# Kernel tuning notes

Hardware: AMD Instinct MI355X
Metric: run time of the kernel (lower is better)

Reference implementation:

```python
import jax, jax.numpy as jnp
import numpy as np

N_HEADS = 8
CLIP = 10.0  # tanh clipping constant of the pointer logits
NEG = -1e9


def setup_inputs() -> dict:
    key = jax.random.key(0)
    ks = jax.random.split(key, 10)
    B, N, H = 1024, 100, 128
    s = 1.0 / np.sqrt(H).astype(np.float32)
    return {
        "encoder_inputs": jax.random.normal(ks[0], (B, N, H), jnp.float32),
        "pool": jax.random.normal(ks[1], (B, H), jnp.float32),
        "capacity": jnp.full((B, 1), 50.0, jnp.float32),  # vehicle capacity
        "demand": (1.0 + 9.0 * jax.random.uniform(ks[2], (B, N), jnp.float32)).at[:, 0].set(0.0),  # depot demand = 0
        "fc_w": jax.random.normal(ks[3], (H, H + 1), jnp.float32) * s,
        "fc1_w": jax.random.normal(ks[4], (H, H), jnp.float32) * s,
        "Wq": jax.random.normal(ks[5], (H, H), jnp.float32) * s,
        "Wk": jax.random.normal(ks[6], (H, H), jnp.float32) * s,
        "Wv": jax.random.normal(ks[7], (H, H), jnp.float32) * s,
        "Wo": jax.random.normal(ks[8], (H, H), jnp.float32) * s,
        "Wk2": jax.random.normal(ks[9], (H, H), jnp.float32) * s,
        "n_steps": 128,
        "T": 1,
        "greedy": 1,
    }


def _decode(encoder_inputs, pool, capacity, demand, fc_w, fc1_w, Wq, Wk, Wv, Wo, Wk2, n_steps, T):
    B, N, H = encoder_inputs.shape
    hd = H // N_HEADS
    # encoder projections are step-invariant -> hoist out of the loop
    K = (encoder_inputs @ Wk.T).reshape(B, N, N_HEADS, hd)
    V = (encoder_inputs @ Wv.T).reshape(B, N, N_HEADS, hd)
    K2 = encoder_inputs @ Wk2.T  # [B, N, H] pointer keys
    pool_proj = pool @ fc1_w.T   # [B, H]
    base_cap = capacity[0, 0]
    rows = jnp.arange(B)

    def update_mask(cap, index, mask1):
        # mask1: permanently visited customers (depot never permanently masked)
        go_depot = (index == 0)
        mask1 = mask1.at[rows, index].set(1.0)
        mask1 = mask1.at[:, 0].set(0.0)
        mask = jnp.maximum(mask1, (demand > cap).astype(jnp.float32))
        # cannot stay at depot; but depot must stay open once all customers are masked
        all_cust = jnp.all(mask[:, 1:] > 0.0, axis=1)
        depot = jnp.where(all_cust, 0.0, go_depot.astype(jnp.float32))
        mask = mask.at[:, 0].set(depot)
        return mask, mask1

    mask0, mask1_0 = update_mask(capacity, jnp.zeros((B,), jnp.int32), jnp.zeros((B, N), jnp.float32))
    inp0 = encoder_inputs[:, 0, :]
    inv_sqrt_hd = 1.0 / jnp.sqrt(jnp.float32(hd))
    inv_sqrt_h = 1.0 / jnp.sqrt(jnp.float32(H))

    def step(carry, _):
        _inp, cap, mask, mask1 = carry
        dec = jnp.concatenate([_inp, cap], axis=-1) @ fc_w.T + pool_proj  # [B, H]
        # multi-head glimpse over encoder nodes
        q = (dec @ Wq.T).reshape(B, N_HEADS, hd)
        scores = jnp.einsum('bhd,bnhd->bhn', q, K) * inv_sqrt_hd
        scores = jnp.where(mask[:, None, :] > 0.0, NEG, scores)
        attn = jax.nn.softmax(scores, axis=-1)
        glimpse = jnp.einsum('bhn,bnhd->bhd', attn, V).reshape(B, H) @ Wo.T
        # single-head clipped pointer logits
        u = CLIP * jnp.tanh(jnp.einsum('bh,bnh->bn', glimpse, K2) * inv_sqrt_h)
        u = jnp.where(mask > 0.0, NEG, u)
        logp_all = jax.nn.log_softmax(u / T, axis=-1)
        index = jnp.argmax(logp_all, axis=-1)  # greedy decoding
        log_p = jnp.take_along_axis(logp_all, index[:, None], axis=1)[:, 0]
        is_done = (jnp.sum(mask1[:, 1:], axis=1) >= N - 1).astype(jnp.float32)
        log_p = log_p * (1.0 - is_done)
        # state update: subtract served demand; reset to base capacity at depot
        sel_d = jnp.take_along_axis(demand, index[:, None], axis=1)
        cap = jnp.where(index[:, None] == 0, base_cap, cap - sel_d)
        mask, mask1 = update_mask(cap, index, mask1)
        _inp = jnp.take_along_axis(encoder_inputs, index[:, None, None], axis=1)[:, 0]
        return (_inp, cap, mask, mask1), (index, log_p)

    _, (actions, log_ps) = jax.lax.scan(step, (inp0, capacity, mask0, mask1_0), None, length=n_steps)
    return actions.T, jnp.sum(log_ps, axis=0)  # ([B, n_steps], [B])


def reference(encoder_inputs, pool, capacity, demand, fc_w, fc1_w, Wq, Wk, Wv, Wo, Wk2, n_steps, T, greedy):
    actions, log_p = _decode(encoder_inputs, pool, capacity, demand, fc_w, fc1_w, Wq, Wk, Wv, Wo, Wk2, n_steps, T)
    return actions, log_p
```

## Files before the change

kernel.cpp:

```cpp
#include <hip/hip_runtime.h>
#include <math.h>

#define NNODE 100
#define NEGV  -1000000000.0f

__device__ float g_Wall [128 * 512];
__device__ float g_Wall2[128 * 128];
__device__ float g_qcap [128];
__device__ float g_C    [(size_t)102400 * 512];
__device__ float g_qpool[(size_t)1024 * 128];
__device__ float g_S1   [(size_t)1024 * 100 * 800];
__device__ float g_Scap [(size_t)1024 * 800];

__device__ __forceinline__ float fast_rcp(float x) { return __builtin_amdgcn_rcpf(x); }
__device__ __forceinline__ float tanh10(float z) {
    const float e2 = __expf(2.0f * z);
    return fmaf(-20.0f, __builtin_amdgcn_rcpf(e2 + 1.0f), 10.0f);
}

template<int CTRL>
__device__ __forceinline__ int dpp_i(int v) {
    return __builtin_amdgcn_update_dpp(0, v, CTRL, 0xF, 0xF, true);
}
template<int CTRL>
__device__ __forceinline__ float dpp_f(float v) {
    return __uint_as_float((unsigned)dpp_i<CTRL>(__float_as_int(v)));
}
__device__ __forceinline__ float swz16_f(float v) {
    return __uint_as_float(
        (unsigned)__builtin_amdgcn_ds_swizzle(__float_as_int(v), 0x401F));
}

__global__ __launch_bounds__(128) void prep_kernel(
    const float* __restrict__ Wk,  const float* __restrict__ Wv,
    const float* __restrict__ Wk2, const float* __restrict__ Wo,
    const float* __restrict__ Wq,  const float* __restrict__ fc_w,
    const float* __restrict__ fc1_w)
{
    const int c = blockIdx.x;
    const int k = threadIdx.x;
    if (c < 128) {
        g_Wall[k * 512 + c] = Wk[c * 128 + k];
    } else if (c < 256) {
        g_Wall[k * 512 + c] = Wv[(c - 128) * 128 + k];
    } else if (c < 384) {
        const int cc = c - 256;
        float acc = 0.f;
        for (int h = 0; h < 128; h++)
            acc = fmaf(Wk2[h * 128 + k], Wo[h * 128 + cc], acc);
        g_Wall[k * 512 + c] = acc;
    } else if (c < 512) {
        const int cc = c - 384;
        float acc = 0.f;
        for (int j = 0; j < 128; j++)
            acc = fmaf(Wq[cc * 128 + j], fc_w[j * 129 + k], acc);
        g_Wall[k * 512 + c] = acc;
    } else if (c == 512) {
        float acc = 0.f;
        for (int j = 0; j < 128; j++)
            acc = fmaf(Wq[k * 128 + j], fc_w[j * 129 + 128], acc);
        g_qcap[k] = acc;
    } else {
        const int cc = c - 513;
        float acc = 0.f;
        for (int j = 0; j < 128; j++)
            acc = fmaf(Wq[cc * 128 + j], fc1_w[j * 128 + k], acc);
        g_Wall2[k * 128 + cc] = acc;
    }
}

__global__ __launch_bounds__(256) void gemm_kernel(const float* __restrict__ A,
                                                   int mode)
{
    const float* __restrict__ W = mode ? g_Wall2 : g_Wall;
    float* __restrict__ C       = mode ? g_qpool : g_C;
    const int ncols             = mode ? 128 : 512;
    const int m0 = blockIdx.x * 128, n0 = blockIdx.y * 128;

    __shared__ __align__(16) float At[32 * 132];
    __shared__ __align__(16) float Ws[32 * 128];
    const int tid = threadIdx.x;
    const int tm = tid >> 5, tn = tid & 31;
    const int mb = tm * 16, nb = tn * 4;
    float4 acc[16];
#pragma unroll
    for (int i = 0; i < 16; i++) acc[i] = make_float4(0.f, 0.f, 0.f, 0.f);

    for (int kc = 0; kc < 4; kc++) {
        for (int f = tid; f < 1024; f += 256) {
            const int r = f >> 3, q8 = f & 7;
            float4 a = *(const float4*)&A[(size_t)(m0 + r) * 128 + kc * 32 + q8 * 4];
            At[(q8 * 4 + 0) * 132 + r] = a.x;
            At[(q8 * 4 + 1) * 132 + r] = a.y;
            At[(q8 * 4 + 2) * 132 + r] = a.z;
            At[(q8 * 4 + 3) * 132 + r] = a.w;
            const int kl = f >> 5, q = f & 31;
            *(float4*)&Ws[kl * 128 + q * 4] =
                *(const float4*)&W[(size_t)(kc * 32 + kl) * ncols + n0 + q * 4];
        }
        __syncthreads();
        for (int k = 0; k < 32; k++) {
            const float4 w = *(float4*)&Ws[k * 128 + nb];
#pragma unroll
            for (int i = 0; i < 16; i += 4) {
                const float4 a = *(float4*)&At[k * 132 + mb + i];
                acc[i + 0].x = fmaf(a.x, w.x, acc[i + 0].x);
                acc[i + 0].y = fmaf(a.x, w.y, acc[i + 0].y);
                acc[i + 0].z = fmaf(a.x, w.z, acc[i + 0].z);
                acc[i + 0].w = fmaf(a.x, w.w, acc[i + 0].w);
                acc[i + 1].x = fmaf(a.y, w.x, acc[i + 1].x);
                acc[i + 1].y = fmaf(a.y, w.y, acc[i + 1].y);
                acc[i + 1].z = fmaf(a.y, w.z, acc[i + 1].z);
                acc[i + 1].w = fmaf(a.y, w.w, acc[i + 1].w);
                acc[i + 2].x = fmaf(a.z, w.x, acc[i + 2].x);
                acc[i + 2].y = fmaf(a.z, w.y, acc[i + 2].y);
                acc[i + 2].z = fmaf(a.z, w.z, acc[i + 2].z);
                acc[i + 2].w = fmaf(a.z, w.w, acc[i + 2].w);
                acc[i + 3].x = fmaf(a.w, w.x, acc[i + 3].x);
                acc[i + 3].y = fmaf(a.w, w.y, acc[i + 3].y);
                acc[i + 3].z = fmaf(a.w, w.z, acc[i + 3].z);
                acc[i + 3].w = fmaf(a.w, w.w, acc[i + 3].w);
            }
        }
        __syncthreads();
    }
#pragma unroll
    for (int i = 0; i < 16; i++)
        *(float4*)&C[(size_t)(m0 + mb + i) * ncols + n0 + nb] = acc[i];
}

__global__ __launch_bounds__(256) void s1_kernel()
{
    const int b = blockIdx.x;
    const int tid = threadIdx.x;
    const int h = tid >> 5, l32 = tid & 31;
    const float* __restrict__ Crow = &g_C[(size_t)b * 100 * 512];

    float4 kr[4][4];
    int nn[4];
#pragma unroll
    for (int j = 0; j < 4; j++) {
        nn[j] = l32 + 32 * j;
#pragma unroll
        for (int i = 0; i < 4; i++) {
            kr[j][i] = (nn[j] < 100)
                ? *(const float4*)&Crow[(size_t)nn[j] * 512 + h * 16 + i * 4]
                : make_float4(0.f, 0.f, 0.f, 0.f);
        }
    }
    float4 qc[4], qp[4];
#pragma unroll
    for (int i = 0; i < 4; i++) {
        qc[i] = *(const float4*)&g_qcap[h * 16 + i * 4];
        qp[i] = *(const float4*)&g_qpool[(size_t)b * 128 + h * 16 + i * 4];
    }
    float sp[4];
#pragma unroll
    for (int j = 0; j < 4; j++) {
        float dc = 0.f, dp = 0.f;
#pragma unroll
        for (int i = 0; i < 4; i++) {
            dc = fmaf(kr[j][i].x, qc[i].x, dc); dc = fmaf(kr[j][i].y, qc[i].y, dc);
            dc = fmaf(kr[j][i].z, qc[i].z, dc); dc = fmaf(kr[j][i].w, qc[i].w, dc);
            dp = fmaf(kr[j][i].x, qp[i].x, dp); dp = fmaf(kr[j][i].y, qp[i].y, dp);
            dp = fmaf(kr[j][i].z, qp[i].z, dp); dp = fmaf(kr[j][i].w, qp[i].w, dp);
        }
        sp[j] = dp;
        if (nn[j] < 100)
            g_Scap[(size_t)b * 800 + h * 100 + nn[j]] = dc * 0.25f;
    }

    float* __restrict__ S1b = &g_S1[(size_t)b * 80000];
#pragma unroll 2
    for (int m = 0; m < 100; m++) {
        float4 q[4];
#pragma unroll
        for (int i = 0; i < 4; i++)
            q[i] = *(const float4*)&Crow[(size_t)m * 512 + 384 + h * 16 + i * 4];
#pragma unroll
        for (int j = 0; j < 4; j++) {
            if (nn[j] < 100) {
                float d = 0.f;
#pragma unroll
                for (int i = 0; i < 4; i++) {
                    d = fmaf(kr[j][i].x, q[i].x, d); d = fmaf(kr[j][i].y, q[i].y, d);
                    d = fmaf(kr[j][i].z, q[i].z, d); d = fmaf(kr[j][i].w, q[i].w, d);
                }
                S1b[(size_t)m * 800 + h * 100 + nn[j]] = (d + sp[j]) * 0.25f;
            }
        }
    }
}

__global__ __launch_bounds__(256) void decode_kernel(
    const float* __restrict__ capacity, const float* __restrict__ demand,
    const int* __restrict__ nsteps_p, const int* __restrict__ T_p,
    float* __restrict__ out)
{
    __shared__ float u_buf[800];
    __shared__ float demand_sh[NNODE];
    __shared__ int   act_sh[512];
    __shared__ int   idx_sh;
    __shared__ float lp_sh;

    const int tid = threadIdx.x;
    const int b   = blockIdx.x;
    const int nsteps = nsteps_p[0];
    const float invT = 1.0f / (float)T_p[0];
    const float base_cap = capacity[0];
    const float inv_sqrt_h = 0.08838834764831845f;

    const float4* __restrict__ C4  = (const float4*)&g_C[(size_t)b * 100 * 512];
    const float*  __restrict__ S1b = &g_S1[(size_t)b * 80000];

    const int w = tid >> 6, l = tid & 63;
    const int g = l >> 3, f = l & 7;
    const int F = 8 * w + f;
    const int h8 = tid >> 5, l32 = tid & 31;

    float4 Vreg[13], K2r[13];
#pragma unroll
    for (int m = 0; m < 13; m++) {
        const int n = g + 8 * m;
        const bool v = n < 100;
        Vreg[m] = v ? C4[(size_t)n * 128 + 32 + F] : make_float4(0.f, 0.f, 0.f, 0.f);
        K2r[m]  = v ? C4[(size_t)n * 128 + 64 + F] : make_float4(0.f, 0.f, 0.f, 0.f);
    }
    float s1r[4], scapr[4], d4[4];
#pragma unroll
    for (int j = 0; j < 4; j++) {
        const int nj = l32 + 32 * j;
        const bool v = nj < 100;
        scapr[j] = v ? g_Scap[(size_t)b * 800 + h8 * 100 + nj] : 0.f;
        s1r[j]   = v ? S1b[h8 * 100 + nj] : 0.f;
        d4[j]    = v ? demand[b * 100 + nj] : 1.0e30f;
    }
    const float de0 = demand[b * 100 + l];
    const float de1 = (l + 64 < 100) ? demand[b * 100 + l + 64] : 1.0e30f;
    for (int n = tid; n < 100; n += 256) demand_sh[n] = demand[b * 100 + n];
    for (int t = tid; t < 512; t += 256) act_sh[t] = 0;
    bool me0 = false, me1 = false;
    unsigned mb4 = 0;
    float cap_r = capacity[b];
    float depot_r;
    {
        const bool am0 = (l == 0) ? true : (de0 > cap_r);
        const bool am1 = (l + 64 >= 100) ? true : (de1 > cap_r);
        depot_r = __all(am0 && am1) ? 0.f : 1.f;
    }
    float logp_r = 0.f;
    int visited_r = 0;
    __syncthreads();

    for (int s = 0; s < nsteps; s++) {
        const float cap = cap_r;

        float a[4];
        float tot;
        {
            float sc[4];
#pragma unroll
            for (int j = 0; j < 4; j++) {
                const int nj = l32 + 32 * j;
                const bool m = (nj == 0) ? (depot_r != 0.f)
                    : (((mb4 >> j) & 1u) || (d4[j] > cap));
                const float raw = fmaf(cap, scapr[j], s1r[j]);
                sc[j] = (nj < 100 && !m) ? raw : NEGV;
            }
#pragma unroll
            for (int j = 0; j < 4; j++) a[j] = __expf(sc[j]);
            tot = (a[0] + a[1]) + (a[2] + a[3]);
        }

        float4 gp4 = make_float4(0.f, 0.f, 0.f, 0.f);
#pragma unroll
        for (int m = 0; m < 13; m++) {
            const int src = ((f >> 2) << 5) | (8 * (m & 3) + g);
            const float av = __shfl(a[m >> 2], src, 64);
            gp4.x = fmaf(av, Vreg[m].x, gp4.x);
            gp4.y = fmaf(av, Vreg[m].y, gp4.y);
            gp4.z = fmaf(av, Vreg[m].z, gp4.z);
            gp4.w = fmaf(av, Vreg[m].w, gp4.w);
        }
        tot += dpp_f<0xB1>(tot);
        tot += dpp_f<0x4E>(tot);
        tot += dpp_f<0x124>(tot);
        tot += dpp_f<0x128>(tot);
        tot += swz16_f(tot);
        gp4.x += dpp_f<0x128>(gp4.x);
        gp4.y += dpp_f<0x128>(gp4.y);
        gp4.z += dpp_f<0x128>(gp4.z);
        gp4.w += dpp_f<0x128>(gp4.w);
        gp4.x += swz16_f(gp4.x);
        gp4.y += swz16_f(gp4.y);
        gp4.z += swz16_f(gp4.z);
        gp4.w += swz16_f(gp4.w);
        gp4.x += __shfl_xor(gp4.x, 32, 64);
        gp4.y += __shfl_xor(gp4.y, 32, 64);
        gp4.z += __shfl_xor(gp4.z, 32, 64);
        gp4.w += __shfl_xor(gp4.w, 32, 64);
        {
            const float th = __shfl(tot, ((f >> 2) << 5) | l32, 64);
            const float rt = fast_rcp(th);
            gp4.x *= rt; gp4.y *= rt; gp4.z *= rt; gp4.w *= rt;
        }

        {
            float pm[13];
#pragma unroll
            for (int m = 0; m < 13; m++) {
                float p = gp4.x * K2r[m].x;
                p = fmaf(gp4.y, K2r[m].y, p);
                p = fmaf(gp4.z, K2r[m].z, p);
                p = fmaf(gp4.w, K2r[m].w, p);
                pm[m] = p;
            }
#pragma unroll
            for (int m = 0; m < 13; m++) pm[m] += dpp_f<0xB1>(pm[m]);
#pragma unroll
            for (int m = 0; m < 13; m++) pm[m] += dpp_f<0x4E>(pm[m]);
            if ((f & 3) == 0) {
                const int r = w * 2 + (f >> 2);
#pragma unroll
                for (int m = 0; m < 13; m++) {
                    const int n = g + 8 * m;
                    if (n < 100) u_buf[r * 100 + n] = pm[m];
                }
            }
        }
        __syncthreads();

        if (w == (s & 3)) {
            float v0, v1 = -3.0e38f;
            {
                float s8 = 0.f;
#pragma unroll
                for (int r = 0; r < 8; r++) s8 += u_buf[r * 100 + l];
                const float u0 = tanh10(s8 * inv_sqrt_h);
                const bool m0 = (l == 0) ? (depot_r != 0.f) : (me0 || de0 > cap);
                v0 = (m0 ? NEGV : u0) * invT;
                if (l + 64 < 100) {
                    float t8 = 0.f;
#pragma unroll
                    for (int r = 0; r < 8; r++) t8 += u_buf[r * 100 + l + 64];
                    const float u1 = tanh10(t8 * inv_sqrt_h);
                    const bool m1 = (me1 || de1 > cap);
                    v1 = (m1 ? NEGV : u1) * invT;
                }
            }
            float tt = __expf(v0) + ((l + 64 < 100) ? __expf(v1) : 0.f);
            float vm = fmaxf(v0, v1);
#define E_STG(CTRL)                                                           \
            {                                                                 \
                tt += dpp_f<CTRL>(tt);                                        \
                vm = fmaxf(vm, dpp_f<CTRL>(vm));                              \
            }
            E_STG(0xB1)
            E_STG(0x4E)
            E_STG(0x124)
            E_STG(0x128)
#undef E_STG
            tt += swz16_f(tt);
            vm = fmaxf(vm, swz16_f(vm));
            tt += __shfl_xor(tt, 32, 64);
            vm = fmaxf(vm, __shfl_xor(vm, 32, 64));
            const unsigned long long b0 = __ballot(v0 == vm);
            const unsigned long long b1 = __ballot(v1 == vm);
            const int idx = b0 ? (int)__builtin_ctzll(b0)
                               : (64 + (int)__builtin_ctzll(b1));
            if (l == 0) {
                idx_sh = idx;
                act_sh[s] = idx;
                lp_sh = (visited_r < 99) ? (vm - __logf(tt)) : 0.f;
            }
        }
        __syncthreads();

        const int idx = idx_sh;
        if (tid == 0) logp_r += lp_sh;

#pragma unroll
        for (int j = 0; j < 4; j++) {
            const int nj = l32 + 32 * j;
            if (nj < 100)
                s1r[j] = S1b[(size_t)idx * 800 + h8 * 100 + nj];
        }

        const float dmd_idx = demand_sh[idx];
        const float capn = (idx == 0) ? base_cap : (cap - dmd_idx);

        visited_r += (idx > 0) ? 1 : 0;
        me0 = me0 || (l == idx && idx > 0);
        me1 = me1 || (l + 64 == idx);
#pragma unroll
        for (int j = 0; j < 4; j++)
            if ((l32 + 32 * j) == idx && idx > 0) mb4 |= (1u << j);

        const bool am0 = (l == 0) ? true : (me0 || de0 > capn);
        const bool am1 = (l + 64 >= 100) ? true : (me1 || de1 > capn);
        const bool allc = __all(am0 && am1);
        depot_r = allc ? 0.f : ((idx == 0) ? 1.f : 0.f);
        cap_r = capn;

        if (visited_r >= 99) break;
    }

    __syncthreads();
    for (int t = tid; t < nsteps; t += 256)
        out[(size_t)b * nsteps + t] = (float)act_sh[t];
    if (tid == 0)
        out[(size_t)gridDim.x * nsteps + b] = logp_r;
}

extern "C" void kernel_launch(void* const* d_in, const int* in_sizes, int n_in,
                              void* d_out, int out_size, void* d_ws, size_t ws_size,
                              hipStream_t stream) {
    const float* enc    = (const float*)d_in[0];
    const float* pool   = (const float*)d_in[1];
    const float* cap    = (const float*)d_in[2];
    const float* demand = (const float*)d_in[3];
    const float* fc_w   = (const float*)d_in[4];
    const float* fc1_w  = (const float*)d_in[5];
    const float* Wq     = (const float*)d_in[6];
    const float* Wk     = (const float*)d_in[7];
    const float* Wv     = (const float*)d_in[8];
    const float* Wo     = (const float*)d_in[9];
    const float* Wk2    = (const float*)d_in[10];
    const int*   nst    = (const int*)d_in[11];
    const int*   Tp     = (const int*)d_in[12];
    float* out = (float*)d_out;

    prep_kernel<<<641, 128, 0, stream>>>(Wk, Wv, Wk2, Wo, Wq, fc_w, fc1_w);
    gemm_kernel<<<dim3(800, 4), 256, 0, stream>>>(enc, 0);
    gemm_kernel<<<dim3(8, 1),   256, 0, stream>>>(pool, 1);
    s1_kernel<<<1024, 256, 0, stream>>>();
    decode_kernel<<<1024, 256, 0, stream>>>(cap, demand, nst, Tp, out);
}
```

Baseline: 888.6 us.

## Remove per-step barrier via redundant argmax in all waves and double-buffered scores

Every wave in the decode loop now does the softmax/argmax reduction redundantly, and u_buf is double-buffered. This removes the second __syncthreads and the shared-memory broadcast of the selected index each step. Cross-lane reductions use permlane16/32 swap builtins where the compiler provides them, falling back to ds_swizzle and shfl otherwise. The s1 kernel also stages the query rows in LDS in two halves instead of reading them from global memory per iteration.

```diff
diff --git a/kernel.cpp b/kernel.cpp
--- a/kernel.cpp
+++ b/kernel.cpp
@@ -26,9 +26,52 @@
 __device__ __forceinline__ float dpp_f(float v) {
     return __uint_as_float((unsigned)dpp_i<CTRL>(__float_as_int(v)));
 }
-__device__ __forceinline__ float swz16_f(float v) {
-    return __uint_as_float(
-        (unsigned)__builtin_amdgcn_ds_swizzle(__float_as_int(v), 0x401F));
+
+#if defined(__has_builtin)
+#  if __has_builtin(__builtin_amdgcn_permlane16_swap)
+#    define HAVE_PL16 1
+#  endif
+#  if __has_builtin(__builtin_amdgcn_permlane32_swap)
+#    define HAVE_PL32 1
+#  endif
+#endif
+
+__device__ __forceinline__ void x16_both(float x, float& a, float& b) {
+#if defined(HAVE_PL16)
+    auto r = __builtin_amdgcn_permlane16_swap(__float_as_uint(x),
+                                              __float_as_uint(x), false, false);
+    a = __uint_as_float(r[0]); b = __uint_as_float(r[1]);
+#else
+    a = x;
+    b = __uint_as_float(
+        (unsigned)__builtin_amdgcn_ds_swizzle(__float_as_int(x), 0x401F));
+#endif
+}
+__device__ __forceinline__ void x32_both(float x, float& a, float& b) {
+#if defined(HAVE_PL32)
+    auto r = __builtin_amdgcn_permlane32_swap(__float_as_uint(x),
+                                              __float_as_uint(x), false, false);
+    a = __uint_as_float(r[0]); b = __uint_as_float(r[1]);
+#else
+    a = x;
+    b = __shfl_xor(x, 32, 64);
+#endif
+}
+__device__ __forceinline__ float x16_sum(float x) { float a, b; x16_both(x, a, b); return a + b; }
+__device__ __forceinline__ float x16_max(float x) { float a, b; x16_both(x, a, b); return fmaxf(a, b); }
+__device__ __forceinline__ float x32_sum(float x) { float a, b; x32_both(x, a, b); return a + b; }
+__device__ __forceinline__ float x32_max(float x) { float a, b; x32_both(x, a, b); return fmaxf(a, b); }
+__device__ __forceinline__ void x32_pair(float x, float& lo, float& hi) {
+#if defined(HAVE_PL32)
+    auto r = __builtin_amdgcn_permlane32_swap(__float_as_uint(x),
+                                              __float_as_uint(x), false, false);
+    lo = __uint_as_float(r[0]); hi = __uint_as_float(r[1]);
+#else
+    const float o = __shfl_xor(x, 32, 64);
+    const bool high = (threadIdx.x & 32) != 0;
+    lo = high ? o : x;
+    hi = high ? x : o;
+#endif
 }
 
 __global__ __launch_bounds__(128) void prep_kernel(
@@ -136,6 +179,8 @@
     const int h = tid >> 5, l32 = tid & 31;
     const float* __restrict__ Crow = &g_C[(size_t)b * 100 * 512];
 
+    __shared__ __align__(16) float Q1sh[50 * 128];
+
     float4 kr[4][4];
     int nn[4];
 #pragma unroll
@@ -171,24 +216,34 @@
     }
 
     float* __restrict__ S1b = &g_S1[(size_t)b * 80000];
-#pragma unroll 2
-    for (int m = 0; m < 100; m++) {
-        float4 q[4];
-#pragma unroll
-        for (int i = 0; i < 4; i++)
-            q[i] = *(const float4*)&Crow[(size_t)m * 512 + 384 + h * 16 + i * 4];
-#pragma unroll
-        for (int j = 0; j < 4; j++) {
-            if (nn[j] < 100) {
-                float d = 0.f;
-#pragma unroll
-                for (int i = 0; i < 4; i++) {
-                    d = fmaf(kr[j][i].x, q[i].x, d); d = fmaf(kr[j][i].y, q[i].y, d);
-                    d = fmaf(kr[j][i].z, q[i].z, d); d = fmaf(kr[j][i].w, q[i].w, d);
+    for (int half = 0; half < 2; half++) {
+        const int mbase = half * 50;
+        for (int f = tid; f < 1600; f += 256) {
+            const int n = f >> 5, c4 = f & 31;
+            *(float4*)&Q1sh[n * 128 + c4 * 4] =
+                *(const float4*)&Crow[(size_t)(mbase + n) * 512 + 384 + c4 * 4];
+        }
+        __syncthreads();
+        for (int mm = 0; mm < 50; mm++) {
+            const int m = mbase + mm;
+            float4 q[4];
+#pragma unroll
+            for (int i = 0; i < 4; i++)
+                q[i] = *(float4*)&Q1sh[mm * 128 + h * 16 + i * 4];
+#pragma unroll
+            for (int j = 0; j < 4; j++) {
+                if (nn[j] < 100) {
+                    float d = 0.f;
+#pragma unroll
+                    for (int i = 0; i < 4; i++) {
+                        d = fmaf(kr[j][i].x, q[i].x, d); d = fmaf(kr[j][i].y, q[i].y, d);
+                        d = fmaf(kr[j][i].z, q[i].z, d); d = fmaf(kr[j][i].w, q[i].w, d);
+                    }
+                    S1b[(size_t)m * 800 + h * 100 + nn[j]] = (d + sp[j]) * 0.25f;
                 }
-                S1b[(size_t)m * 800 + h * 100 + nn[j]] = (d + sp[j]) * 0.25f;
-            }
-        }
+            }
+        }
+        __syncthreads();
     }
 }
 
@@ -197,11 +252,9 @@
     const int* __restrict__ nsteps_p, const int* __restrict__ T_p,
     float* __restrict__ out)
 {
-    __shared__ float u_buf[800];
+    __shared__ float u_buf[2 * 800];
     __shared__ float demand_sh[NNODE];
     __shared__ int   act_sh[512];
-    __shared__ int   idx_sh;
-    __shared__ float lp_sh;
 
     const int tid = threadIdx.x;
     const int b   = blockIdx.x;
@@ -250,6 +303,7 @@
     }
     float logp_r = 0.f;
     int visited_r = 0;
+    int ub = 0;
     __syncthreads();
 
     for (int s = 0; s < nsteps; s++) {
@@ -286,21 +340,23 @@
         tot += dpp_f<0x4E>(tot);
         tot += dpp_f<0x124>(tot);
         tot += dpp_f<0x128>(tot);
-        tot += swz16_f(tot);
+        tot = x16_sum(tot);
         gp4.x += dpp_f<0x128>(gp4.x);
         gp4.y += dpp_f<0x128>(gp4.y);
         gp4.z += dpp_f<0x128>(gp4.z);
         gp4.w += dpp_f<0x128>(gp4.w);
-        gp4.x += swz16_f(gp4.x);
-        gp4.y += swz16_f(gp4.y);
-        gp4.z += swz16_f(gp4.z);
-        gp4.w += swz16_f(gp4.w);
-        gp4.x += __shfl_xor(gp4.x, 32, 64);
-        gp4.y += __shfl_xor(gp4.y, 32, 64);
-        gp4.z += __shfl_xor(gp4.z, 32, 64);
-        gp4.w += __shfl_xor(gp4.w, 32, 64);
+        gp4.x = x16_sum(gp4.x);
+        gp4.y = x16_sum(gp4.y);
+        gp4.z = x16_sum(gp4.z);
+        gp4.w = x16_sum(gp4.w);
+        gp4.x = x32_sum(gp4.x);
+        gp4.y = x32_sum(gp4.y);
+        gp4.z = x32_sum(gp4.z);
+        gp4.w = x32_sum(gp4.w);
         {
-            const float th = __shfl(tot, ((f >> 2) << 5) | l32, 64);
+            float tlo, thi;
+            x32_pair(tot, tlo, thi);
+            const float th = (f >> 2) ? thi : tlo;
             const float rt = fast_rcp(th);
             gp4.x *= rt; gp4.y *= rt; gp4.z *= rt; gp4.w *= rt;
         }
@@ -324,60 +380,49 @@
 #pragma unroll
                 for (int m = 0; m < 13; m++) {
                     const int n = g + 8 * m;
-                    if (n < 100) u_buf[r * 100 + n] = pm[m];
+                    if (n < 100) u_buf[ub + r * 100 + n] = pm[m];
                 }
             }
         }
         __syncthreads();
 
-        if (w == (s & 3)) {
-            float v0, v1 = -3.0e38f;
-            {
-                float s8 = 0.f;
-#pragma unroll
-                for (int r = 0; r < 8; r++) s8 += u_buf[r * 100 + l];
-                const float u0 = tanh10(s8 * inv_sqrt_h);
-                const bool m0 = (l == 0) ? (depot_r != 0.f) : (me0 || de0 > cap);
-                v0 = (m0 ? NEGV : u0) * invT;
-                if (l + 64 < 100) {
-                    float t8 = 0.f;
-#pragma unroll
-                    for (int r = 0; r < 8; r++) t8 += u_buf[r * 100 + l + 64];
-                    const float u1 = tanh10(t8 * inv_sqrt_h);
-                    const bool m1 = (me1 || de1 > cap);
-                    v1 = (m1 ? NEGV : u1) * invT;
-                }
-            }
-            float tt = __expf(v0) + ((l + 64 < 100) ? __expf(v1) : 0.f);
-            float vm = fmaxf(v0, v1);
+        float v0, v1 = -3.0e38f;
+        {
+            float s8 = 0.f;
+#pragma unroll
+            for (int r = 0; r < 8; r++) s8 += u_buf[ub + r * 100 + l];
+            const float u0 = tanh10(s8 * inv_sqrt_h);
+            const bool m0 = (l == 0) ? (depot_r != 0.f) : (me0 || de0 > cap);
+            v0 = (m0 ? NEGV : u0) * invT;
+            if (l + 64 < 100) {
+                float t8 = 0.f;
+#pragma unroll
+                for (int r = 0; r < 8; r++) t8 += u_buf[ub + r * 100 + l + 64];
+                const float u1 = tanh10(t8 * inv_sqrt_h);
+                const bool m1 = (me1 || de1 > cap);
+                v1 = (m1 ? NEGV : u1) * invT;
+            }
+        }
+        float tt = __expf(v0) + ((l + 64 < 100) ? __expf(v1) : 0.f);
+        float vm = fmaxf(v0, v1);
 #define E_STG(CTRL)                                                           \
-            {                                                                 \
-                tt += dpp_f<CTRL>(tt);                                        \
-                vm = fmaxf(vm, dpp_f<CTRL>(vm));                              \
-            }
-            E_STG(0xB1)
-            E_STG(0x4E)
-            E_STG(0x124)
-            E_STG(0x128)
+        {                                                                     \
+            tt += dpp_f<CTRL>(tt);                                            \
+            vm = fmaxf(vm, dpp_f<CTRL>(vm));                                  \
+        }
+        E_STG(0xB1)
+        E_STG(0x4E)
+        E_STG(0x124)
+        E_STG(0x128)
 #undef E_STG
-            tt += swz16_f(tt);
-            vm = fmaxf(vm, swz16_f(vm));
-            tt += __shfl_xor(tt, 32, 64);
-            vm = fmaxf(vm, __shfl_xor(vm, 32, 64));
-            const unsigned long long b0 = __ballot(v0 == vm);
-            const unsigned long long b1 = __ballot(v1 == vm);
-            const int idx = b0 ? (int)__builtin_ctzll(b0)
-                               : (64 + (int)__builtin_ctzll(b1));
-            if (l == 0) {
-                idx_sh = idx;
-                act_sh[s] = idx;
-                lp_sh = (visited_r < 99) ? (vm - __logf(tt)) : 0.f;
-            }
-        }
-        __syncthreads();
-
-        const int idx = idx_sh;
-        if (tid == 0) logp_r += lp_sh;
+        tt = x16_sum(tt);
+        vm = x16_max(vm);
+        tt = x32_sum(tt);
+        vm = x32_max(vm);
+        const unsigned long long b0 = __ballot(v0 == vm);
+        const unsigned long long b1 = __ballot(v1 == vm);
+        const int idx = b0 ? (int)__builtin_ctzll(b0)
+                           : (64 + (int)__builtin_ctzll(b1));
 
 #pragma unroll
         for (int j = 0; j < 4; j++) {
@@ -389,6 +434,7 @@
         const float dmd_idx = demand_sh[idx];
         const float capn = (idx == 0) ? base_cap : (cap - dmd_idx);
 
+        if (visited_r < 99) logp_r += vm - __logf(tt);
         visited_r += (idx > 0) ? 1 : 0;
         me0 = me0 || (l == idx && idx > 0);
         me1 = me1 || (l + 64 == idx);
@@ -401,6 +447,8 @@
         const bool allc = __all(am0 && am1);
         depot_r = allc ? 0.f : ((idx == 0) ? 1.f : 0.f);
         cap_r = capn;
+        if (tid == 0) act_sh[s] = idx;
+        ub ^= 800;
 
         if (visited_r >= 99) break;
     }
@@ -424,8 +472,8 @@
     const float* Wq     = (const float*)d_in[6];
     const float* Wk     = (const float*)d_in[7];
     const float* Wv     = (const float*)d_in[8];
+    const float* Wk2    = (const float*)d_in[10];
     const float* Wo     = (const float*)d_in[9];
-    const float* Wk2    = (const float*)d_in[10];
     const int*   nst    = (const int*)d_in[11];
     const int*   Tp     = (const int*)d_in[12];
     float* out = (float*)d_out;
```

Result: faster. 839.9 us (-5.5%).
